# Kernel optimization log

Hardware: AMD Instinct MI355X
Metric: run time of the kernel (lower is better)

## Reference

```python
import jax, jax.numpy as jnp
import numpy as np

EPS = 1e-5  # torch LayerNorm default


def setup_inputs() -> dict:
    key = jax.random.key(0)
    ks = jax.random.split(key, 12)
    N, D, F = 4096, 1024, 4096
    s = 1.0 / np.sqrt(D)
    sf = 1.0 / np.sqrt(F)
    return {
        "embeddings": jax.random.normal(ks[0], (N, D), dtype=jnp.float32),
        "Wq": jax.random.normal(ks[1], (D, D), dtype=jnp.float32) * s,
        "bq": jnp.zeros((D,), jnp.float32),
        "Wk": jax.random.normal(ks[2], (D, D), dtype=jnp.float32) * s,
        "bk": jnp.zeros((D,), jnp.float32),
        "Wv": jax.random.normal(ks[3], (D, D), dtype=jnp.float32) * s,
        "bv": jnp.zeros((D,), jnp.float32),
        "gamma": jnp.ones((D,), jnp.float32),
        "beta": jnp.zeros((D,), jnp.float32),
        "W1": jax.random.normal(ks[4], (D, F), dtype=jnp.float32) * s,
        "b1": jnp.zeros((F,), jnp.float32),
        "W2": jax.random.normal(ks[5], (F, D), dtype=jnp.float32) * sf,
        "b2": jnp.zeros((D,), jnp.float32),
    }


def reference(embeddings, Wq, bq, Wk, bk, Wv, bv, gamma, beta, W1, b1, W2, b2):
    N, D = embeddings.shape
    scale = jnp.sqrt(jnp.float32(D))  # embed_dim ** 0.5
    Q = embeddings @ Wq + bq          # [N, D]
    K = embeddings @ Wk + bk
    V = embeddings @ Wv + bv
    attn = (Q @ K.T) / scale          # [N, N]
    # causal mask: strictly upper triangle -> -inf
    causal = jnp.tril(jnp.ones((N, N), dtype=bool))
    attn = jnp.where(causal, attn, -jnp.inf)
    A = jax.nn.softmax(attn, axis=-1)
    attn_emb = A @ V                  # [N, D]  (dropout = identity at eval)
    # add & norm (LayerNorm over last dim)
    x = attn_emb + embeddings
    mu = jnp.mean(x, axis=-1, keepdims=True)
    var = jnp.mean((x - mu) ** 2, axis=-1, keepdims=True)
    x = (x - mu) / jnp.sqrt(var + EPS) * gamma + beta
    # FFN (no residual after ff in the original module)
    h = jax.nn.relu(x @ W1 + b1)
    return h @ W2 + b2
```

## Files before the change

### kernel.cpp

```cpp
#include <hip/hip_runtime.h>
#include <stdint.h>


using short8 = __attribute__((ext_vector_type(8))) short;
using f32x4  = __attribute__((ext_vector_type(4))) float;

__device__ __forceinline__ uint16_t f2bf(float f) {
  uint32_t u = __builtin_bit_cast(uint32_t, f);
  u += 0x7FFFu + ((u >> 16) & 1u);
  return (uint16_t)(u >> 16);
}

__device__ __forceinline__ float bf2f(uint16_t u) {
  return __builtin_bit_cast(float, (uint32_t)u << 16);
}

__device__ __forceinline__ void gload_lds16(const uint16_t* g, uint16_t* l) {
  __builtin_amdgcn_global_load_lds(
      (__attribute__((address_space(1))) void*)(void*)g,
      (__attribute__((address_space(3))) void*)l, 16, 0, 0);
}


__global__ __launch_bounds__(256) void gemm_qkv(
    const uint16_t* __restrict__ A, const uint16_t* __restrict__ Bt,
    const float* __restrict__ bias, uint16_t* __restrict__ Cout,
    uint16_t* __restrict__ Vt)
{
  constexpr int BK = 64;
  __shared__ uint16_t As[128 * BK];
  __shared__ uint16_t Bs[128 * BK];
  int id = blockIdx.x;
  int x = id & 7, t = id >> 3;
  int bn = x * 3 + t % 3;
  int bm = t / 3;
  bool vblk = (bn >= 16);

  int tid  = threadIdx.x;
  int lane = tid & 63;
  int wave = tid >> 6;
  int wm = (wave >> 1) * 64, wn = (wave & 1) * 64;
  int lr = lane & 15, quad = lane >> 4;

  const uint16_t *Ag[4], *Bg[4];
  uint16_t *Al[4], *Bl[4];
#pragma unroll
  for (int s = 0; s < 4; ++s) {
    int c = tid + 256 * s;
    int r = c >> 3, q = (c & 7) ^ (r & 7);
    Ag[s] = A  + (size_t)(bm * 128 + r) * 1024 + q * 8;
    Bg[s] = Bt + (size_t)(bn * 128 + r) * 1024 + q * 8;
    Al[s] = As + c * 8;
    Bl[s] = Bs + c * 8;
  }
  const uint16_t* Fa = vblk ? Bs : As;
  const uint16_t* Fb = vblk ? As : Bs;

  f32x4 acc[4][4] = {};

  for (int k0 = 0; k0 < 1024; k0 += BK) {
    __syncthreads();
#pragma unroll
    for (int s = 0; s < 4; ++s) gload_lds16(Ag[s] + k0, Al[s]);
#pragma unroll
    for (int s = 0; s < 4; ++s) gload_lds16(Bg[s] + k0, Bl[s]);
    __syncthreads();
#pragma unroll
    for (int h = 0; h < 2; ++h) {
      short8 af[4], bfr[4];
      int cc = quad + 4 * h;
#pragma unroll
      for (int i = 0; i < 4; ++i) {
        int r = wm + i * 16 + lr;
        af[i] = *(const short8*)(&Fa[(r * 8 + (cc ^ (r & 7))) * 8]);
      }
#pragma unroll
      for (int j = 0; j < 4; ++j) {
        int r = wn + j * 16 + lr;
        bfr[j] = *(const short8*)(&Fb[(r * 8 + (cc ^ (r & 7))) * 8]);
      }
#pragma unroll
      for (int i = 0; i < 4; ++i)
#pragma unroll
        for (int j = 0; j < 4; ++j)
          acc[i][j] = __builtin_amdgcn_mfma_f32_16x16x32_bf16(af[i], bfr[j], acc[i][j], 0, 0, 0);
    }
  }

  if (vblk) {
#pragma unroll
    for (int i = 0; i < 4; ++i) {
#pragma unroll
      for (int r = 0; r < 4; ++r) {
        int n = bn * 128 + wm + i * 16 + quad * 4 + r;
        float bv = bias[n];
        uint16_t* dst = Vt + (size_t)(n - 2048) * 4096 + bm * 128;
#pragma unroll
        for (int j = 0; j < 4; ++j)
          dst[wn + j * 16 + lr] = f2bf(acc[i][j][r] + bv);
      }
    }
  } else {
    int row0 = bm * 128 + wm + quad * 4;
    int col0 = bn * 128 + wn + lr;
#pragma unroll
    for (int j = 0; j < 4; ++j) {
      int col = col0 + j * 16;
      float bv = bias[col];
#pragma unroll
      for (int i = 0; i < 4; ++i)
#pragma unroll
        for (int r = 0; r < 4; ++r)
          Cout[(size_t)(row0 + i * 16 + r) * 3072 + col] = f2bf(acc[i][j][r] + bv);
    }
  }
}

__global__ __launch_bounds__(256) void gemm_ffn1(
    const uint16_t* __restrict__ A, const uint16_t* __restrict__ Bt,
    const float* __restrict__ bias, uint16_t* __restrict__ Cout)
{
  constexpr int BK = 64;
  __shared__ uint16_t As[128 * BK];
  __shared__ uint16_t Bs[128 * BK];
  int id = blockIdx.x;
  int bn = (id & 7) * 4 + ((id >> 3) & 3);
  int bm = id >> 5;

  int tid  = threadIdx.x;
  int lane = tid & 63;
  int wave = tid >> 6;
  int wm = (wave >> 1) * 64, wn = (wave & 1) * 64;
  int lr = lane & 15, quad = lane >> 4;

  const uint16_t *Ag[4], *Bg[4];
  uint16_t *Al[4], *Bl[4];
#pragma unroll
  for (int s = 0; s < 4; ++s) {
    int c = tid + 256 * s;
    int r = c >> 3, q = (c & 7) ^ (r & 7);
    Ag[s] = A  + (size_t)(bm * 128 + r) * 1024 + q * 8;
    Bg[s] = Bt + (size_t)(bn * 128 + r) * 1024 + q * 8;
    Al[s] = As + c * 8;
    Bl[s] = Bs + c * 8;
  }

  f32x4 acc[4][4] = {};

  for (int k0 = 0; k0 < 1024; k0 += BK) {
    __syncthreads();
#pragma unroll
    for (int s = 0; s < 4; ++s) gload_lds16(Ag[s] + k0, Al[s]);
#pragma unroll
    for (int s = 0; s < 4; ++s) gload_lds16(Bg[s] + k0, Bl[s]);
    __syncthreads();
#pragma unroll
    for (int h = 0; h < 2; ++h) {
      short8 af[4], bfr[4];
      int cc = quad + 4 * h;
#pragma unroll
      for (int i = 0; i < 4; ++i) {
        int r = wm + i * 16 + lr;
        af[i] = *(const short8*)(&As[(r * 8 + (cc ^ (r & 7))) * 8]);
      }
#pragma unroll
      for (int j = 0; j < 4; ++j) {
        int r = wn + j * 16 + lr;
        bfr[j] = *(const short8*)(&Bs[(r * 8 + (cc ^ (r & 7))) * 8]);
      }
#pragma unroll
      for (int i = 0; i < 4; ++i)
#pragma unroll
        for (int j = 0; j < 4; ++j)
          acc[i][j] = __builtin_amdgcn_mfma_f32_16x16x32_bf16(af[i], bfr[j], acc[i][j], 0, 0, 0);
    }
  }

  int row0 = bm * 128 + wm + quad * 4;
  int col0 = bn * 128 + wn + lr;
#pragma unroll
  for (int j = 0; j < 4; ++j) {
    int col = col0 + j * 16;
    float bv = bias[col];
#pragma unroll
    for (int i = 0; i < 4; ++i)
#pragma unroll
      for (int r = 0; r < 4; ++r)
        Cout[(size_t)(row0 + i * 16 + r) * 4096 + col] =
            f2bf(fmaxf(acc[i][j][r] + bv, 0.0f));
  }
}

__global__ __launch_bounds__(256) void gemm_s(
    const uint16_t* __restrict__ Qm, const uint16_t* __restrict__ Km,
    uint16_t* __restrict__ Sb, float* __restrict__ lvec,
    int lda, int ldb, int ldc, float scale)
{
  constexpr int BK = 64;
  __shared__ uint16_t As[64 * BK];
  __shared__ uint16_t Bs[128 * BK];
  int id = blockIdx.x;
  int i64 = id & 63, bn = id >> 6;
  if (bn > (i64 >> 1)) return;

  int tid  = threadIdx.x;
  int lane = tid & 63;
  int wave = tid >> 6;
  int wm = (wave >> 1) * 32, wn = (wave & 1) * 64;
  int lr = lane & 15, quad = lane >> 4;

  const uint16_t *Ag[2], *Bg[4];
  uint16_t *Al[2], *Bl[4];
#pragma unroll
  for (int s = 0; s < 2; ++s) {
    int c = tid + 256 * s;
    int r = c >> 3, q = (c & 7) ^ (r & 7);
    Ag[s] = Qm + (size_t)(i64 * 64 + r) * lda + q * 8;
    Al[s] = As + c * 8;
  }
#pragma unroll
  for (int s = 0; s < 4; ++s) {
    int c = tid + 256 * s;
    int r = c >> 3, q = (c & 7) ^ (r & 7);
    Bg[s] = Km + (size_t)(bn * 128 + r) * ldb + q * 8;
    Bl[s] = Bs + c * 8;
  }

  f32x4 acc[2][4] = {};

  for (int k0 = 0; k0 < 1024; k0 += BK) {
    __syncthreads();
#pragma unroll
    for (int s = 0; s < 2; ++s) gload_lds16(Ag[s] + k0, Al[s]);
#pragma unroll
    for (int s = 0; s < 4; ++s) gload_lds16(Bg[s] + k0, Bl[s]);
    __syncthreads();
#pragma unroll
    for (int h = 0; h < 2; ++h) {
      short8 af[2], bfr[4];
      int cc = quad + 4 * h;
#pragma unroll
      for (int i = 0; i < 2; ++i) {
        int r = wm + i * 16 + lr;
        af[i] = *(const short8*)(&As[(r * 8 + (cc ^ (r & 7))) * 8]);
      }
#pragma unroll
      for (int j = 0; j < 4; ++j) {
        int r = wn + j * 16 + lr;
        bfr[j] = *(const short8*)(&Bs[(r * 8 + (cc ^ (r & 7))) * 8]);
      }
#pragma unroll
      for (int i = 0; i < 2; ++i)
#pragma unroll
        for (int j = 0; j < 4; ++j)
          acc[i][j] = __builtin_amdgcn_mfma_f32_16x16x32_bf16(af[i], bfr[j], acc[i][j], 0, 0, 0);
    }
  }

  int row0 = i64 * 64 + wm + quad * 4;
  int col0 = bn * 128 + wn + lr;
#pragma unroll
  for (int i = 0; i < 2; ++i) {
#pragma unroll
    for (int r = 0; r < 4; ++r) {
      int row = row0 + i * 16 + r;
      float s = 0.0f;
#pragma unroll
      for (int j = 0; j < 4; ++j) {
        int col = col0 + j * 16;
        float v = (col <= row) ? __expf(acc[i][j][r] * scale) : 0.0f;
        Sb[(size_t)row * ldc + col] = f2bf(v);
        s += v;
      }
#pragma unroll
      for (int o = 8; o > 0; o >>= 1) s += __shfl_xor(s, o, 64);
      if (lr == 0) unsafeAtomicAdd(&lvec[row], s);
    }
  }
}

__global__ __launch_bounds__(256) void gemm_o(
    const uint16_t* __restrict__ Sb, const uint16_t* __restrict__ Vt,
    uint16_t* __restrict__ Opart)
{
  constexpr int BK = 64;
  __shared__ uint16_t As[128 * BK];
  __shared__ uint16_t Bs[128 * BK];
  int id = blockIdx.x;
  int bn = id / 80, p = id % 80;
  int c, bm;
  if      (p < 25) { c = 0; bm = 7 + p; }
  else if (p < 49) { c = 1; bm = 8 + (p - 25); }
  else if (p < 65) { c = 2; bm = 16 + (p - 49); }
  else if (p < 73) { c = 3; bm = 24 + (p - 65); }
  else             { c = 0; bm = 79 - p; }
  int klo = c << 10;
  int khi = (bm + 1) << 7; if (khi > ((c + 1) << 10)) khi = (c + 1) << 10;

  int tid  = threadIdx.x;
  int lane = tid & 63;
  int wave = tid >> 6;
  int wm = (wave >> 1) * 64, wn = (wave & 1) * 64;
  int lr = lane & 15, quad = lane >> 4;

  const uint16_t *Ag[4], *Bg[4];
  uint16_t *Al[4], *Bl[4];
#pragma unroll
  for (int s = 0; s < 4; ++s) {
    int cch = tid + 256 * s;
    int r = cch >> 3, q = (cch & 7) ^ (r & 7);
    Ag[s] = Sb + (size_t)(bm * 128 + r) * 4096 + q * 8;
    Bg[s] = Vt + (size_t)(bn * 128 + r) * 4096 + q * 8;
    Al[s] = As + cch * 8;
    Bl[s] = Bs + cch * 8;
  }

  f32x4 acc[4][4] = {};

  for (int k0 = klo; k0 < khi; k0 += BK) {
    __syncthreads();
#pragma unroll
    for (int s = 0; s < 4; ++s) gload_lds16(Ag[s] + k0, Al[s]);
#pragma unroll
    for (int s = 0; s < 4; ++s) gload_lds16(Bg[s] + k0, Bl[s]);
    __syncthreads();
#pragma unroll
    for (int h = 0; h < 2; ++h) {
      short8 af[4], bfr[4];
      int cc = quad + 4 * h;
#pragma unroll
      for (int i = 0; i < 4; ++i) {
        int r = wm + i * 16 + lr;
        af[i] = *(const short8*)(&As[(r * 8 + (cc ^ (r & 7))) * 8]);
      }
#pragma unroll
      for (int j = 0; j < 4; ++j) {
        int r = wn + j * 16 + lr;
        bfr[j] = *(const short8*)(&Bs[(r * 8 + (cc ^ (r & 7))) * 8]);
      }
#pragma unroll
      for (int i = 0; i < 4; ++i)
#pragma unroll
        for (int j = 0; j < 4; ++j)
          acc[i][j] = __builtin_amdgcn_mfma_f32_16x16x32_bf16(af[i], bfr[j], acc[i][j], 0, 0, 0);
    }
  }

  uint16_t* P = Opart + (size_t)c * 4194304;
  int row0 = bm * 128 + wm + quad * 4;
  int col0 = bn * 128 + wn + lr;
#pragma unroll
  for (int j = 0; j < 4; ++j)
#pragma unroll
    for (int i = 0; i < 4; ++i)
#pragma unroll
      for (int r = 0; r < 4; ++r)
        P[(size_t)(row0 + i * 16 + r) * 1024 + col0 + j * 16] = f2bf(acc[i][j][r]);
}

__global__ __launch_bounds__(256) void gemm_ffn2(
    const uint16_t* __restrict__ A, const uint16_t* __restrict__ Bt,
    const float* __restrict__ bias, float* __restrict__ Cout)
{
  constexpr int BK = 64;
  __shared__ uint16_t As[64 * BK];
  __shared__ uint16_t Bs[64 * BK];
  int id = blockIdx.x;
  int bn = id >> 6, bm = id & 63;

  int tid  = threadIdx.x;
  int lane = tid & 63;
  int wave = tid >> 6;
  int wm = (wave >> 1) * 32, wn = (wave & 1) * 32;
  int lr = lane & 15, quad = lane >> 4;

  const uint16_t *Ag[2], *Bg[2];
  uint16_t *Al[2], *Bl[2];
#pragma unroll
  for (int s = 0; s < 2; ++s) {
    int c = tid + 256 * s;
    int r = c >> 3, q = (c & 7) ^ (r & 7);
    Ag[s] = A  + (size_t)(bm * 64 + r) * 4096 + q * 8;
    Bg[s] = Bt + (size_t)(bn * 64 + r) * 4096 + q * 8;
    Al[s] = As + c * 8;
    Bl[s] = Bs + c * 8;
  }

  f32x4 acc[2][2] = {};

  for (int k0 = 0; k0 < 4096; k0 += BK) {
    __syncthreads();
#pragma unroll
    for (int s = 0; s < 2; ++s) gload_lds16(Ag[s] + k0, Al[s]);
#pragma unroll
    for (int s = 0; s < 2; ++s) gload_lds16(Bg[s] + k0, Bl[s]);
    __syncthreads();
#pragma unroll
    for (int h = 0; h < 2; ++h) {
      short8 af[2], bfr[2];
      int cc = quad + 4 * h;
#pragma unroll
      for (int i = 0; i < 2; ++i) {
        int r = wm + i * 16 + lr;
        af[i] = *(const short8*)(&As[(r * 8 + (cc ^ (r & 7))) * 8]);
      }
#pragma unroll
      for (int j = 0; j < 2; ++j) {
        int r = wn + j * 16 + lr;
        bfr[j] = *(const short8*)(&Bs[(r * 8 + (cc ^ (r & 7))) * 8]);
      }
#pragma unroll
      for (int i = 0; i < 2; ++i)
#pragma unroll
        for (int j = 0; j < 2; ++j)
          acc[i][j] = __builtin_amdgcn_mfma_f32_16x16x32_bf16(af[i], bfr[j], acc[i][j], 0, 0, 0);
    }
  }

  int row0 = bm * 64 + wm + quad * 4;
  int col0 = bn * 64 + wn + lr;
#pragma unroll
  for (int j = 0; j < 2; ++j) {
    int col = col0 + j * 16;
    float bv = bias[col];
#pragma unroll
    for (int i = 0; i < 2; ++i)
#pragma unroll
      for (int r = 0; r < 4; ++r)
        Cout[(size_t)(row0 + i * 16 + r) * 1024 + col] = acc[i][j][r] + bv;
  }
}

__device__ __forceinline__ float block_sum(float v, float* red) {
#pragma unroll
  for (int o = 32; o > 0; o >>= 1) v += __shfl_xor(v, o, 64);
  if ((threadIdx.x & 63) == 0) red[threadIdx.x >> 6] = v;
  __syncthreads();
  v = red[0] + red[1] + red[2] + red[3];
  __syncthreads();
  return v;
}

__global__ __launch_bounds__(256) void add_layernorm(
    const uint16_t* __restrict__ P, const float* __restrict__ l,
    const float* __restrict__ emb, const float* __restrict__ gamma,
    const float* __restrict__ beta, uint16_t* __restrict__ xB)
{
  __shared__ float red[4];
  int i = blockIdx.x, tid = threadIdx.x;
  float inv_l = 1.0f / l[i];
  int nc = (i >> 10) + 1;
  float s0 = 0.0f, s1 = 0.0f, s2 = 0.0f, s3 = 0.0f;
  for (int c = 0; c < nc; ++c) {
    ushort4 a = ((const ushort4*)(P + (size_t)c * 4194304 + (size_t)i * 1024))[tid];
    s0 += bf2f(a.x); s1 += bf2f(a.y); s2 += bf2f(a.z); s3 += bf2f(a.w);
  }
  float4 b = ((const float4*)(emb + (size_t)i * 1024))[tid];
  float x0 = s0 * inv_l + b.x, x1 = s1 * inv_l + b.y;
  float x2 = s2 * inv_l + b.z, x3 = s3 * inv_l + b.w;
  float mu = block_sum(x0 + x1 + x2 + x3, red) * (1.0f / 1024.0f);
  float d0 = x0 - mu, d1 = x1 - mu, d2 = x2 - mu, d3 = x3 - mu;
  float var = block_sum(d0 * d0 + d1 * d1 + d2 * d2 + d3 * d3, red) * (1.0f / 1024.0f);
  float rs = rsqrtf(var + 1e-5f);
  float4 g  = ((const float4*)gamma)[tid];
  float4 be = ((const float4*)beta)[tid];
  ushort4 o;
  o.x = f2bf(d0 * rs * g.x + be.x);
  o.y = f2bf(d1 * rs * g.y + be.y);
  o.z = f2bf(d2 * rs * g.z + be.z);
  o.w = f2bf(d3 * rs * g.w + be.w);
  ((ushort4*)(xB + (size_t)i * 1024))[tid] = o;
}

__global__ __launch_bounds__(256) void prep(
    const float* __restrict__ emb, const float* __restrict__ Wq,
    const float* __restrict__ Wk, const float* __restrict__ Wv,
    const float* __restrict__ W1, const float* __restrict__ W2,
    const float* __restrict__ bq, const float* __restrict__ bk,
    const float* __restrict__ bv, uint16_t* __restrict__ embB,
    uint16_t* __restrict__ WqkvT, uint16_t* __restrict__ W1T,
    uint16_t* __restrict__ W2T, float* __restrict__ bqkv,
    float* __restrict__ lvec)
{
  __shared__ float tile[32][33];
  int b = blockIdx.x, tid = threadIdx.x;
  if (b < 4096) {
    int idx = b * 256 + tid;
    float4 v = ((const float4*)emb)[idx];
    ushort4 o; o.x = f2bf(v.x); o.y = f2bf(v.y); o.z = f2bf(v.z); o.w = f2bf(v.w);
    ((ushort4*)embB)[idx] = o;
    return;
  }
  int tx = tid & 31, ty = tid >> 5;
  if (b < 7168) {
    int local = b - 4096;
    const float* in = (local < 1024) ? Wq : (local < 2048) ? Wk : Wv;
    uint16_t* o = WqkvT + (size_t)(local >> 10) * 1048576;
    int rem = local & 1023;
    int r0 = (rem >> 5) * 32, c0 = (rem & 31) * 32;
#pragma unroll
    for (int r = 0; r < 32; r += 8)
      tile[ty + r][tx] = in[(size_t)(r0 + ty + r) * 1024 + c0 + tx];
    __syncthreads();
#pragma unroll
    for (int r = 0; r < 32; r += 8)
      o[(size_t)(c0 + ty + r) * 1024 + r0 + tx] = f2bf(tile[tx][ty + r]);
    return;
  }
  if (b < 11264) {
    int local = b - 7168;
    int c0 = (local & 127) * 32, r0 = (local >> 7) * 32;
#pragma unroll
    for (int r = 0; r < 32; r += 8)
      tile[ty + r][tx] = W1[(size_t)(r0 + ty + r) * 4096 + c0 + tx];
    __syncthreads();
#pragma unroll
    for (int r = 0; r < 32; r += 8)
      W1T[(size_t)(c0 + ty + r) * 1024 + r0 + tx] = f2bf(tile[tx][ty + r]);
    return;
  }
  if (b < 15360) {
    int local = b - 11264;
    int c0 = (local & 31) * 32, r0 = (local >> 5) * 32;
#pragma unroll
    for (int r = 0; r < 32; r += 8)
      tile[ty + r][tx] = W2[(size_t)(r0 + ty + r) * 1024 + c0 + tx];
    __syncthreads();
#pragma unroll
    for (int r = 0; r < 32; r += 8)
      W2T[(size_t)(c0 + ty + r) * 4096 + r0 + tx] = f2bf(tile[tx][ty + r]);
    return;
  }
  if (b < 15372) {
    int i = (b - 15360) * 256 + tid;
    bqkv[i] = (i < 1024) ? bq[i] : (i < 2048) ? bk[i - 1024] : bv[i - 2048];
    return;
  }
  {
#pragma unroll
    for (int i = tid; i < 4096; i += 256) lvec[i] = 0.0f;
  }
}

extern "C" void kernel_launch(void* const* d_in, const int* in_sizes, int n_in,
                              void* d_out, int out_size, void* d_ws, size_t ws_size,
                              hipStream_t stream) {
  const float* emb   = (const float*)d_in[0];
  const float* Wq    = (const float*)d_in[1];
  const float* bq    = (const float*)d_in[2];
  const float* Wk    = (const float*)d_in[3];
  const float* bk    = (const float*)d_in[4];
  const float* Wv    = (const float*)d_in[5];
  const float* bv    = (const float*)d_in[6];
  const float* gamma = (const float*)d_in[7];
  const float* beta  = (const float*)d_in[8];
  const float* W1    = (const float*)d_in[9];
  const float* b1    = (const float*)d_in[10];
  const float* W2    = (const float*)d_in[11];
  const float* b2    = (const float*)d_in[12];

  char* w = (char*)d_ws;
  const size_t MB = 1ull << 20;
  uint16_t* embB  = (uint16_t*)(w + 0 * MB);
  uint16_t* WqkvT = (uint16_t*)(w + 8 * MB);
  uint16_t* W1T   = (uint16_t*)(w + 14 * MB);
  uint16_t* W2T   = (uint16_t*)(w + 22 * MB);
  float*    bqkv  = (float*)(w + 30 * MB);
  float*    lvec  = (float*)(w + 30 * MB + 65536);
  uint16_t* QKVb  = (uint16_t*)(w + 31 * MB);
  uint16_t* Vt    = (uint16_t*)(w + 55 * MB);
  uint16_t* Sb    = (uint16_t*)(w + 63 * MB);
  uint16_t* hB    = (uint16_t*)(w + 63 * MB);
  uint16_t* Opart = (uint16_t*)(w + 95 * MB);
  uint16_t* xB    = (uint16_t*)(w + 0 * MB);

  prep<<<15373, 256, 0, stream>>>(emb, Wq, Wk, Wv, W1, W2, bq, bk, bv,
                                  embB, WqkvT, W1T, W2T, bqkv, lvec);

  gemm_qkv<<<768, 256, 0, stream>>>(embB, WqkvT, bqkv, QKVb, Vt);
  const uint16_t* Qb = QKVb;
  const uint16_t* Kb = QKVb + 1024;

  gemm_s<<<2048, 256, 0, stream>>>(Qb, Kb, Sb, lvec, 3072, 3072, 4096, 0.03125f);

  gemm_o<<<640, 256, 0, stream>>>(Sb, Vt, Opart);

  add_layernorm<<<4096, 256, 0, stream>>>(Opart, lvec, emb, gamma, beta, xB);

  gemm_ffn1<<<1024, 256, 0, stream>>>(xB, W1T, b1, hB);

  gemm_ffn2<<<1024, 256, 0, stream>>>(hB, W2T, b2, (float*)d_out);
}
```

Baseline: 317.6 us.

## Use intra-block split-K with larger M tile in FFN2 GEMM

The FFN2 GEMM now uses 512-thread blocks split into two 4-wave groups. Each group handles half of K (2048) on a 128x64 output tile, and the partial sums are reduced through LDS before the bias is added and the result stored. This is meant to increase A/B tile reuse and in-block parallelism on the long K=4096 dimension, cutting global loads per output. In exchange it adds an LDS reduction epilogue, uses more LDS and registers, and launches fewer blocks (512).

```diff
diff --git a/kernel.cpp b/kernel.cpp
--- a/kernel.cpp
+++ b/kernel.cpp
@@ -358,76 +358,106 @@
         P[(size_t)(row0 + i * 16 + r) * 1024 + col0 + j * 16] = f2bf(acc[i][j][r]);
 }
 
-__global__ __launch_bounds__(256) void gemm_ffn2(
+__global__ __launch_bounds__(512) void gemm_ffn2(
     const uint16_t* __restrict__ A, const uint16_t* __restrict__ Bt,
     const float* __restrict__ bias, float* __restrict__ Cout)
 {
   constexpr int BK = 64;
-  __shared__ uint16_t As[64 * BK];
-  __shared__ uint16_t Bs[64 * BK];
+  __shared__ char ldsbuf[49152];
   int id = blockIdx.x;
-  int bn = id >> 6, bm = id & 63;
-
-  int tid  = threadIdx.x;
-  int lane = tid & 63;
-  int wave = tid >> 6;
-  int wm = (wave >> 1) * 32, wn = (wave & 1) * 32;
+  int bn = id >> 5, bm = id & 31;
+
+  int tid   = threadIdx.x;
+  int lane  = tid & 63;
+  int wave  = tid >> 6;
+  int group = wave >> 2;
+  int wave4 = wave & 3;
+  int gtid  = tid & 255;
+  int wm = (wave4 >> 1) * 64, wn = (wave4 & 1) * 32;
   int lr = lane & 15, quad = lane >> 4;
 
-  const uint16_t *Ag[2], *Bg[2];
-  uint16_t *Al[2], *Bl[2];
+  uint16_t* Ag_l = (uint16_t*)ldsbuf + group * 8192;
+  uint16_t* Bg_l = (uint16_t*)(ldsbuf + 32768) + group * 4096;
+  int kbase = group * 2048;
+
+  const uint16_t *Ag[4], *Bg[2];
+  uint16_t *Al[4], *Bl[2];
+#pragma unroll
+  for (int s = 0; s < 4; ++s) {
+    int c = gtid + 256 * s;
+    int r = c >> 3, q = (c & 7) ^ (r & 7);
+    Ag[s] = A + (size_t)(bm * 128 + r) * 4096 + kbase + q * 8;
+    Al[s] = Ag_l + c * 8;
+  }
 #pragma unroll
   for (int s = 0; s < 2; ++s) {
-    int c = tid + 256 * s;
+    int c = gtid + 256 * s;
     int r = c >> 3, q = (c & 7) ^ (r & 7);
-    Ag[s] = A  + (size_t)(bm * 64 + r) * 4096 + q * 8;
-    Bg[s] = Bt + (size_t)(bn * 64 + r) * 4096 + q * 8;
-    Al[s] = As + c * 8;
-    Bl[s] = Bs + c * 8;
-  }
-
-  f32x4 acc[2][2] = {};
-
-  for (int k0 = 0; k0 < 4096; k0 += BK) {
-    __syncthreads();
-#pragma unroll
-    for (int s = 0; s < 2; ++s) gload_lds16(Ag[s] + k0, Al[s]);
+    Bg[s] = Bt + (size_t)(bn * 64 + r) * 4096 + kbase + q * 8;
+    Bl[s] = Bg_l + c * 8;
+  }
+
+  f32x4 acc[4][2] = {};
+
+  for (int k0 = 0; k0 < 2048; k0 += BK) {
+    __syncthreads();
+#pragma unroll
+    for (int s = 0; s < 4; ++s) gload_lds16(Ag[s] + k0, Al[s]);
 #pragma unroll
     for (int s = 0; s < 2; ++s) gload_lds16(Bg[s] + k0, Bl[s]);
     __syncthreads();
 #pragma unroll
     for (int h = 0; h < 2; ++h) {
-      short8 af[2], bfr[2];
+      short8 af[4], bfr[2];
       int cc = quad + 4 * h;
 #pragma unroll
-      for (int i = 0; i < 2; ++i) {
+      for (int i = 0; i < 4; ++i) {
         int r = wm + i * 16 + lr;
-        af[i] = *(const short8*)(&As[(r * 8 + (cc ^ (r & 7))) * 8]);
+        af[i] = *(const short8*)(&Ag_l[(r * 8 + (cc ^ (r & 7))) * 8]);
       }
 #pragma unroll
       for (int j = 0; j < 2; ++j) {
         int r = wn + j * 16 + lr;
-        bfr[j] = *(const short8*)(&Bs[(r * 8 + (cc ^ (r & 7))) * 8]);
-      }
-#pragma unroll
-      for (int i = 0; i < 2; ++i)
+        bfr[j] = *(const short8*)(&Bg_l[(r * 8 + (cc ^ (r & 7))) * 8]);
+      }
+#pragma unroll
+      for (int i = 0; i < 4; ++i)
 #pragma unroll
         for (int j = 0; j < 2; ++j)
           acc[i][j] = __builtin_amdgcn_mfma_f32_16x16x32_bf16(af[i], bfr[j], acc[i][j], 0, 0, 0);
     }
   }
 
-  int row0 = bm * 64 + wm + quad * 4;
-  int col0 = bn * 64 + wn + lr;
-#pragma unroll
-  for (int j = 0; j < 2; ++j) {
-    int col = col0 + j * 16;
-    float bv = bias[col];
-#pragma unroll
-    for (int i = 0; i < 2; ++i)
-#pragma unroll
-      for (int r = 0; r < 4; ++r)
-        Cout[(size_t)(row0 + i * 16 + r) * 1024 + col] = acc[i][j][r] + bv;
+  __syncthreads();
+  float* Lf = (float*)ldsbuf;
+  if (group == 1) {
+#pragma unroll
+    for (int i = 0; i < 4; ++i)
+#pragma unroll
+      for (int r = 0; r < 4; ++r) {
+        int lrow = wm + i * 16 + quad * 4 + r;
+#pragma unroll
+        for (int j = 0; j < 2; ++j)
+          Lf[lrow * 65 + wn + j * 16 + lr] = acc[i][j][r];
+      }
+  }
+  __syncthreads();
+  if (group == 0) {
+    int row0 = bm * 128 + wm + quad * 4;
+    int col0 = bn * 64 + wn + lr;
+#pragma unroll
+    for (int j = 0; j < 2; ++j) {
+      int col = col0 + j * 16;
+      float bv = bias[col];
+#pragma unroll
+      for (int i = 0; i < 4; ++i)
+#pragma unroll
+        for (int r = 0; r < 4; ++r) {
+          int lrow = wm + i * 16 + quad * 4 + r;
+          Cout[(size_t)(row0 + i * 16 + r) * 1024 + col] =
+              acc[i][j][r] + Lf[lrow * 65 + wn + j * 16 + lr] + bv;
+        }
+    }
   }
 }
 
@@ -589,5 +619,5 @@
 
   gemm_ffn1<<<1024, 256, 0, stream>>>(xB, W1T, b1, hB);
 
-  gemm_ffn2<<<1024, 256, 0, stream>>>(hB, W2T, b2, (float*)d_out);
-}
+  gemm_ffn2<<<512, 512, 0, stream>>>(hB, W2T, b2, (float*)d_out);
+}
```

Result: faster. 308.3 us (-2.9%).
